# Kernel optimization log

Measured on AMD Instinct MI355X. Metric: run time of the kernel, lower is better.

The kernel has to match this reference:

```python
import jax, jax.numpy as jnp
import numpy as np

B, L, D, H = 1, 2048, 1024, 16
d = D // H  # head dim = 64


def setup_inputs() -> dict:
    key = jax.random.key(0)
    ks = jax.random.split(key, 8)
    s = 1.0 / np.sqrt(D)
    return {
        "x": jax.random.normal(ks[0], (B, L, D), jnp.float32),
        "Wqkv_w": (jax.random.normal(ks[1], (D, 3 * D), jnp.float32) * s),
        "Wqkv_b": jnp.zeros((3 * D,), jnp.float32),
        "out_w": (jax.random.normal(ks[2], (D, D), jnp.float32) * s),
        "out_b": jnp.zeros((D,), jnp.float32),
        "W_static": jnp.zeros((H, d, d), jnp.float32),
        "Lambda_raw": jax.random.uniform(ks[3], (H, d, d), jnp.float32, -3.0, 3.0),
        "Gamma": jax.random.uniform(ks[4], (H, d, d), jnp.float32, -0.5 / np.sqrt(d), 0.5 / np.sqrt(d)),
        "gate_w1": (jax.random.normal(ks[5], (D, D // 2), jnp.float32) * s),
        "gate_b1": jnp.zeros((D // 2,), jnp.float32),
        "gate_w2": (jax.random.normal(ks[6], (D // 2, H), jnp.float32) * (1.0 / np.sqrt(D // 2))),
        "gate_b2": jnp.zeros((H,), jnp.float32),
    }


def _forward(x, Wqkv_w, Wqkv_b, out_w, out_b, W_static, Lambda_raw, Gamma,
             gate_w1, gate_b1, gate_w2, gate_b2):
    Bb, Ll, Dm = x.shape
    Hh = Gamma.shape[0]
    dd = Dm // Hh
    scale = 1.0 / np.sqrt(dd)

    # qkv projection: (B,L,3D) -> (3, B, H, L, d) layout
    qkv = (x @ Wqkv_w + Wqkv_b).reshape(Bb, Ll, 3, Hh, dd)
    q = jnp.transpose(qkv[:, :, 0], (0, 2, 1, 3))  # (B,H,L,d)
    k = jnp.transpose(qkv[:, :, 1], (0, 2, 1, 3))
    v = jnp.transpose(qkv[:, :, 2], (0, 2, 1, 3))

    # --- softmax branch (causal, additive -10000 mask like the original) ---
    scores = jnp.einsum('bhid,bhjd->bhij', q, k) * scale
    causal_mask = jnp.triu(jnp.full((Ll, Ll), -10000.0, dtype=scores.dtype), 1)
    attn = jax.nn.softmax(scores + causal_mask, axis=-1)
    y_softmax = jnp.einsum('bhij,bhjd->bhid', attn, v)

    # --- STP branch: linear recurrence over time via lax.scan ---
    retention = 1.0 - jax.nn.sigmoid(Lambda_raw)  # (H,d,d)
    k_stp = k * scale

    def step(state, inp):
        q_t, k_t, v_t = inp  # each (B,H,d)
        hebbian = v_t[..., :, None] * k_t[..., None, :]          # (B,H,d,d)
        state = retention * state + Gamma * hebbian              # (B,H,d,d)
        y_t = jnp.einsum('bhij,bhj->bhi', W_static + state, q_t)  # (B,H,d)
        return state, y_t

    state0 = jnp.zeros((Bb, Hh, dd, dd), x.dtype)
    qT = jnp.moveaxis(q, 2, 0)      # (L,B,H,d)
    kT = jnp.moveaxis(k_stp, 2, 0)
    vT = jnp.moveaxis(v, 2, 0)
    _, ys = jax.lax.scan(step, state0, (qT, kT, vT))
    y_stp = jnp.moveaxis(ys, 0, 2)  # (B,H,L,d)

    # --- learned gate: Linear -> GELU(exact) -> Linear -> sigmoid ---
    g = jax.nn.gelu(x @ gate_w1 + gate_b1, approximate=False)
    alpha = jax.nn.sigmoid(g @ gate_w2 + gate_b2)        # (B,L,H)
    alpha = jnp.transpose(alpha, (0, 2, 1))[..., None]   # (B,H,L,1)

    y = alpha * y_softmax + (1.0 - alpha) * y_stp        # (B,H,L,d)
    y = jnp.transpose(y, (0, 2, 1, 3)).reshape(Bb, Ll, Dm)
    return y @ out_w + out_b


def reference(x, Wqkv_w, Wqkv_b, out_w, out_b, W_static, Lambda_raw, Gamma,
              gate_w1, gate_b1, gate_w2, gate_b2):
    return _forward(x, Wqkv_w, Wqkv_b, out_w, out_b, W_static, Lambda_raw,
                    Gamma, gate_w1, gate_b1, gate_w2, gate_b2)
```

## Files before the change

### kernel.cpp

```cpp
#include <hip/hip_runtime.h>
#include <hip/hip_bf16.h>

#define L_SEQ 2048
#define DMODEL 1024
#define NHEAD 16
#define DHEAD 64
#define D3 3072

typedef __attribute__((ext_vector_type(8))) short s8v;
typedef __attribute__((ext_vector_type(4))) float f4v;
typedef unsigned int u32;
#define AS1 __attribute__((address_space(1)))
#define AS3 __attribute__((address_space(3)))

__device__ __forceinline__ short f2bf(float f) {
  __hip_bfloat16 h = __float2bfloat16(f);
  return *reinterpret_cast<short*>(&h);
}
__device__ __forceinline__ int pack2bf(float lo, float hi) {
  return (int)(((unsigned)(unsigned short)f2bf(hi) << 16) |
               (unsigned)(unsigned short)f2bf(lo));
}

__global__ __launch_bounds__(256) void conv_x(const float* __restrict__ x,
                                              short* __restrict__ xb)
{
  int i = (blockIdx.x * 256 + threadIdx.x) * 4;
  float4 v = *(const float4*)(x + i);
  short4 o;
  o.x = f2bf(v.x); o.y = f2bf(v.y); o.z = f2bf(v.z); o.w = f2bf(v.w);
  *(short4*)(xb + i) = o;
}

__global__ __launch_bounds__(256) void transpose_conv(const float* __restrict__ W,
    short* __restrict__ Wt, int K, int N)
{
  __shared__ float T[32][33];
  int bx = blockIdx.x, by = blockIdx.y;
  int col = threadIdx.x & 31, rb = threadIdx.x >> 5;
  #pragma unroll
  for (int it = 0; it < 4; ++it) {
    int r = it * 8 + rb;
    T[r][col] = W[(size_t)(by * 32 + r) * N + bx * 32 + col];
  }
  __syncthreads();
  #pragma unroll
  for (int it = 0; it < 4; ++it) {
    int r = it * 8 + rb;
    Wt[(size_t)(bx * 32 + r) * K + by * 32 + col] = f2bf(T[col][r]);
  }
}

__global__ __launch_bounds__(256) void conv_qkv(const float* __restrict__ qkv,
    short* __restrict__ Qb, short* __restrict__ Kb, short* __restrict__ Vtb)
{
  int kb = blockIdx.x, h = blockIdx.y;
  int tid = threadIdx.x;
  __shared__ float Vs[64][65];
  for (int idx = tid; idx < 2048; idx += 256) {
    int key = idx >> 5, e2 = idx & 31;
    size_t base = (size_t)(kb * 64 + key) * D3 + h * 64 + e2 * 2;
    float2 qv = *(const float2*)(qkv + base);
    float2 kv = *(const float2*)(qkv + base + 1024);
    float2 vv = *(const float2*)(qkv + base + 2048);
    size_t o = ((size_t)h * 2048 + kb * 64 + key) * 64 + e2 * 2;
    *(int*)&Qb[o] = pack2bf(qv.x, qv.y);
    *(int*)&Kb[o] = pack2bf(kv.x, kv.y);
    Vs[key][e2 * 2] = vv.x; Vs[key][e2 * 2 + 1] = vv.y;
  }
  __syncthreads();
  for (int idx = tid; idx < 2048; idx += 256) {
    int dim = idx >> 5, k2 = idx & 31;
    *(int*)&Vtb[((size_t)h * 64 + dim) * 2048 + kb * 64 + k2 * 2] =
        pack2bf(Vs[k2 * 2][dim], Vs[k2 * 2 + 1][dim]);
  }
}

template<int BM, int BN, int MODE>
__global__ __launch_bounds__(256) void gemm_mfma(
    const short* __restrict__ A, const short* __restrict__ Bt,
    const float* __restrict__ bias, const float* __restrict__ bias2,
    float* __restrict__ C, short* __restrict__ C2,
    int M, int N, int K)
{
  constexpr int LA = BM / 64, LB = BN / 64;
  constexpr int WM = BM / 2, WN = BN / 2;
  constexpr int MT = WM / 16, NT = WN / 16;
  __shared__ __align__(16) short As[2][BM * 32];
  __shared__ __align__(16) short Bs[2][BN * 32];
  const int tid = threadIdx.x;
  const int w = tid >> 6, lane = tid & 63;
  const int quad = lane >> 4, c = lane & 15;
  const int m0 = blockIdx.y * BM, n0 = blockIdx.x * BN;
  const int wm = (w & 1) * WM, wn = (w >> 1) * WN;
  f4v acc[MT][NT] = {};

  auto stage = [&](int buf, int k0) {
    #pragma unroll
    for (int it = 0; it < LA; ++it) {
      int off = (it * 256 + tid) * 16;
      int row = off >> 6, colh = (off & 63) >> 1;
      __builtin_amdgcn_global_load_lds(
          (const AS1 u32*)(A + (size_t)(m0 + row) * K + k0 + colh),
          (AS3 u32*)(&As[buf][0] + (off >> 1)), 16, 0, 0);
    }
    #pragma unroll
    for (int it = 0; it < LB; ++it) {
      int off = (it * 256 + tid) * 16;
      int row = off >> 6, colh = (off & 63) >> 1;
      __builtin_amdgcn_global_load_lds(
          (const AS1 u32*)(Bt + (size_t)(n0 + row) * K + k0 + colh),
          (AS3 u32*)(&Bs[buf][0] + (off >> 1)), 16, 0, 0);
    }
  };
  stage(0, 0);
  int cur = 0;
  for (int k0 = 0; k0 < K; k0 += 32) {
    __syncthreads();
    if (k0 + 32 < K) stage(cur ^ 1, k0 + 32);
    s8v af[MT], bf[NT];
    #pragma unroll
    for (int mt = 0; mt < MT; ++mt)
      af[mt] = *(s8v*)&As[cur][(wm + mt * 16 + c) * 32 + quad * 8];
    #pragma unroll
    for (int nt = 0; nt < NT; ++nt)
      bf[nt] = *(s8v*)&Bs[cur][(wn + nt * 16 + c) * 32 + quad * 8];
    #pragma unroll
    for (int mt = 0; mt < MT; ++mt)
      #pragma unroll
      for (int nt = 0; nt < NT; ++nt)
        acc[mt][nt] = __builtin_amdgcn_mfma_f32_16x16x32_bf16(
            af[mt], bf[nt], acc[mt][nt], 0, 0, 0);
    cur ^= 1;
  }
  #pragma unroll
  for (int mt = 0; mt < MT; ++mt)
    #pragma unroll
    for (int r = 0; r < 4; ++r) {
      int m = m0 + wm + mt * 16 + quad * 4 + r;
      #pragma unroll
      for (int nt = 0; nt < NT; ++nt) {
        int n = n0 + wn + nt * 16 + c;
        float v = acc[mt][nt][r];
        if (MODE == 0) {
          C[(size_t)m * N + n] = v + bias[n];
        } else {
          if (n < 3072) {
            C[(size_t)m * 3072 + n] = v + bias[n];
          } else {
            float t = v + bias2[n - 3072];
            t = 0.5f * t * (1.0f + erff(t * 0.70710678118654752f));
            C2[(size_t)m * 512 + (n - 3072)] = f2bf(t);
          }
        }
      }
    }
}

__global__ __launch_bounds__(256) void attn_mfma(
    const short* __restrict__ Qb, const short* __restrict__ Kb,
    const short* __restrict__ Vtb, float* __restrict__ ysm)
{
  const int bid = blockIdx.x;
  const int h  = bid & 15;
  const int qt = bid >> 4;
  const int q0 = qt * 64;
  const int nt = qt + 1;
  const int tid = threadIdx.x;
  const int w = tid >> 6, lane = tid & 63;
  const int quad = lane >> 4, c = lane & 15;

  __shared__ __align__(16) char smem[27648];
  short* Ks = (short*)smem;
  short* Vt = Ks + 4608;
  short* Ps = Vt + 4608;
  float* Ob = (float*)smem;

  const int qrow = q0 + w * 16 + c;
  s8v qf[2];
  qf[0] = *(const s8v*)(Qb + ((size_t)h * 2048 + qrow) * 64 + quad * 8);
  qf[1] = *(const s8v*)(Qb + ((size_t)h * 2048 + qrow) * 64 + 32 + quad * 8);

  const int srow = tid >> 3, sc = (tid & 7) * 8;
  int4 pk0, pk1, pv0, pv1;
  auto load_tile = [&](int t0) {
    const short* kbase = Kb + ((size_t)h * 2048 + t0 * 64) * 64;
    const short* vbase = Vtb + (size_t)h * 64 * 2048 + t0 * 64;
    pk0 = *(const int4*)(kbase + (size_t)srow * 64 + sc);
    pk1 = *(const int4*)(kbase + (size_t)(srow + 32) * 64 + sc);
    pv0 = *(const int4*)(vbase + (size_t)srow * 2048 + sc);
    pv1 = *(const int4*)(vbase + (size_t)(srow + 32) * 2048 + sc);
  };
  load_tile(0);

  f4v o_acc[4] = {};
  float m = -1e30f, l = 0.f;

  for (int t0 = 0; t0 < nt; ++t0) {
    __syncthreads();
    *(int4*)&Ks[srow * 72 + sc] = pk0;
    *(int4*)&Ks[(srow + 32) * 72 + sc] = pk1;
    *(int4*)&Vt[srow * 72 + sc] = pv0;
    *(int4*)&Vt[(srow + 32) * 72 + sc] = pv1;
    __syncthreads();
    if (t0 + 1 < nt) load_tile(t0 + 1);

    f4v s_acc[4] = {};
    #pragma unroll
    for (int kt = 0; kt < 4; ++kt) {
      #pragma unroll
      for (int kc = 0; kc < 2; ++kc) {
        s8v kf = *(s8v*)&Ks[(kt * 16 + c) * 72 + kc * 32 + quad * 8];
        s_acc[kt] = __builtin_amdgcn_mfma_f32_16x16x32_bf16(kf, qf[kc], s_acc[kt], 0, 0, 0);
      }
    }
    float sv[4][4];
    bool full = (t0 * 64 + 63) <= (q0 + w * 16);
    #pragma unroll
    for (int kt = 0; kt < 4; ++kt)
      #pragma unroll
      for (int r = 0; r < 4; ++r) {
        float s = s_acc[kt][r] * 0.125f;
        if (!full) {
          int key = t0 * 64 + kt * 16 + quad * 4 + r;
          s = (key <= qrow) ? s : -1e30f;
        }
        sv[kt][r] = s;
      }
    float mloc = -1e30f;
    #pragma unroll
    for (int kt = 0; kt < 4; ++kt)
      #pragma unroll
      for (int r = 0; r < 4; ++r) mloc = fmaxf(mloc, sv[kt][r]);
    mloc = fmaxf(mloc, __shfl_xor(mloc, 16));
    mloc = fmaxf(mloc, __shfl_xor(mloc, 32));
    float mnew = fmaxf(m, mloc);
    float alpha = __expf(m - mnew);
    m = mnew;
    float p[4][4], ls = 0.f;
    #pragma unroll
    for (int kt = 0; kt < 4; ++kt)
      #pragma unroll
      for (int r = 0; r < 4; ++r) { p[kt][r] = __expf(sv[kt][r] - mnew); ls += p[kt][r]; }
    ls += __shfl_xor(ls, 16);
    ls += __shfl_xor(ls, 32);
    l = l * alpha + ls;
    #pragma unroll
    for (int mt = 0; mt < 4; ++mt)
      #pragma unroll
      for (int r = 0; r < 4; ++r) o_acc[mt][r] *= alpha;
    short* Pw = Ps + w * 1152;
    #pragma unroll
    for (int kt = 0; kt < 4; ++kt) {
      *(int*)&Pw[c * 72 + kt * 16 + quad * 4]     = pack2bf(p[kt][0], p[kt][1]);
      *(int*)&Pw[c * 72 + kt * 16 + quad * 4 + 2] = pack2bf(p[kt][2], p[kt][3]);
    }
    #pragma unroll
    for (int kc2 = 0; kc2 < 2; ++kc2) {
      s8v pf = *(s8v*)&Pw[c * 72 + kc2 * 32 + quad * 8];
      #pragma unroll
      for (int mt = 0; mt < 4; ++mt) {
        s8v vf = *(s8v*)&Vt[(mt * 16 + c) * 72 + kc2 * 32 + quad * 8];
        o_acc[mt] = __builtin_amdgcn_mfma_f32_16x16x32_bf16(vf, pf, o_acc[mt], 0, 0, 0);
      }
    }
  }

  float rinv = 1.f / l;
  __syncthreads();
  #pragma unroll
  for (int mt = 0; mt < 4; ++mt)
    #pragma unroll
    for (int r = 0; r < 4; ++r)
      Ob[(w * 16 + c) * 66 + mt * 16 + quad * 4 + r] = o_acc[mt][r] * rinv;
  __syncthreads();
  for (int i = tid; i < 4096; i += 256) {
    int q = i >> 6, e = i & 63;
    ysm[((size_t)h * L_SEQ + q0 + q) * 64 + e] = Ob[q * 66 + e];
  }
}

__global__ __launch_bounds__(256) void stp_local(const float* __restrict__ qkv,
    const float* __restrict__ Lam, const float* __restrict__ Gam,
    float* __restrict__ states)
{
  int c = blockIdx.x, h = blockIdx.y;
  int tid = threadIdx.x;
  int i = tid >> 2, j0 = (tid & 3) * 16;
  __shared__ float Kc[64][64];
  __shared__ float Vc[64][64];
  for (int idx = tid; idx < 64 * 64; idx += 256) {
    int t = idx >> 6, e = idx & 63;
    size_t base = (size_t)(c * 64 + t) * D3 + h * 64 + e;
    Kc[t][e] = qkv[base + 1024] * 0.125f;
    Vc[t][e] = qkv[base + 2048];
  }
  float r[16], g[16], s[16];
  #pragma unroll
  for (int e = 0; e < 16; ++e) {
    int idx = h * 4096 + i * 64 + j0 + e;
    float lam = Lam[idx];
    r[e] = 1.f / (1.f + expf(lam));
    g[e] = Gam[idx];
    s[e] = 0.f;
  }
  __syncthreads();
  for (int t = 0; t < 64; ++t) {
    float v = Vc[t][i];
    #pragma unroll
    for (int e = 0; e < 16; ++e)
      s[e] = r[e] * s[e] + g[e] * (v * Kc[t][j0 + e]);
  }
  #pragma unroll
  for (int e = 0; e < 16; ++e)
    states[((size_t)h * 32 + c) * 4096 + i * 64 + j0 + e] = s[e];
}

__global__ __launch_bounds__(256) void stp_scan(const float* __restrict__ Lam,
                                                float* __restrict__ states)
{
  int gid = blockIdx.x * 256 + threadIdx.x;
  float lam = Lam[gid];
  float r = 1.f / (1.f + expf(lam));
  float r64 = r;
  #pragma unroll
  for (int q = 0; q < 6; ++q) r64 *= r64;
  int h = gid >> 12, low = gid & 4095;
  float acc = 0.f;
  for (int c = 0; c < 32; ++c) {
    size_t idx = ((size_t)h * 32 + c) * 4096 + low;
    float dloc = states[idx];
    states[idx] = acc;
    acc = r64 * acc + dloc;
  }
}

__global__ __launch_bounds__(256) void stp_out(const float* __restrict__ qkv,
    const float* __restrict__ Lam, const float* __restrict__ Gam,
    const float* __restrict__ Wst, const float* __restrict__ states,
    float* __restrict__ ystp)
{
  int c = blockIdx.x, h = blockIdx.y;
  int tid = threadIdx.x;
  int i = tid >> 2, j0 = (tid & 3) * 16;
  __shared__ float Kc[64][64];
  __shared__ float Vc[64][64];
  __shared__ float Qc[64][64];
  for (int idx = tid; idx < 64 * 64; idx += 256) {
    int t = idx >> 6, e = idx & 63;
    size_t base = (size_t)(c * 64 + t) * D3 + h * 64 + e;
    Qc[t][e] = qkv[base];
    Kc[t][e] = qkv[base + 1024] * 0.125f;
    Vc[t][e] = qkv[base + 2048];
  }
  float r[16], g[16], s[16], w[16];
  #pragma unroll
  for (int e = 0; e < 16; ++e) {
    int idx = h * 4096 + i * 64 + j0 + e;
    float lam = Lam[idx];
    r[e] = 1.f / (1.f + expf(lam));
    g[e] = Gam[idx];
    w[e] = Wst[idx];
    s[e] = states[((size_t)h * 32 + c) * 4096 + i * 64 + j0 + e];
  }
  __syncthreads();
  for (int t = 0; t < 64; ++t) {
    float v = Vc[t][i];
    float y = 0.f;
    #pragma unroll
    for (int e = 0; e < 16; ++e) {
      s[e] = r[e] * s[e] + g[e] * (v * Kc[t][j0 + e]);
      y += (w[e] + s[e]) * Qc[t][j0 + e];
    }
    y += __shfl_xor(y, 1);
    y += __shfl_xor(y, 2);
    if ((tid & 3) == 0)
      ystp[((size_t)h * L_SEQ + c * 64 + t) * 64 + i] = y;
  }
}

__global__ __launch_bounds__(256) void gate2_kernel(const short* __restrict__ g_bf,
    const float* __restrict__ w2, const float* __restrict__ b2,
    float* __restrict__ alpha)
{
  int gid = blockIdx.x * 256 + threadIdx.x;
  int l = gid >> 4, h = gid & 15;
  float acc = b2[h];
  const short* grow = g_bf + (size_t)l * 512;
  for (int c2 = 0; c2 < 512; c2 += 2) {
    u32 pk = *(const u32*)(grow + c2);
    float g0 = __uint_as_float(pk << 16);
    float g1 = __uint_as_float(pk & 0xffff0000u);
    acc += g0 * w2[c2 * 16 + h] + g1 * w2[(c2 + 1) * 16 + h];
  }
  alpha[gid] = 1.f / (1.f + expf(-acc));
}

__global__ __launch_bounds__(256) void combine_kernel(const float* __restrict__ ysm,
    const float* __restrict__ ystp, const float* __restrict__ alpha,
    short* __restrict__ ycb)
{
  int gid = blockIdx.x * 256 + threadIdx.x;
  int l = gid >> 10, cidx = gid & 1023;
  int h = cidx >> 6, e = cidx & 63;
  float a = alpha[l * 16 + h];
  size_t src = ((size_t)h * L_SEQ + l) * 64 + e;
  ycb[gid] = f2bf(a * ysm[src] + (1.f - a) * ystp[src]);
}

extern "C" void kernel_launch(void* const* d_in, const int* in_sizes, int n_in,
                              void* d_out, int out_size, void* d_ws, size_t ws_size,
                              hipStream_t stream) {
  (void)in_sizes; (void)n_in; (void)out_size; (void)ws_size;
  const float* x      = (const float*)d_in[0];
  const float* Wqkv_w = (const float*)d_in[1];
  const float* Wqkv_b = (const float*)d_in[2];
  const float* out_w  = (const float*)d_in[3];
  const float* out_b  = (const float*)d_in[4];
  const float* W_st   = (const float*)d_in[5];
  const float* Lam    = (const float*)d_in[6];
  const float* Gam    = (const float*)d_in[7];
  const float* gw1    = (const float*)d_in[8];
  const float* gb1    = (const float*)d_in[9];
  const float* gw2    = (const float*)d_in[10];
  const float* gb2    = (const float*)d_in[11];

  float* ws     = (float*)d_ws;
  float* qkv    = ws;
  float* ysm    = ws + 6291456;
  float* ystp   = ws + 8388608;
  float* states = ws + 10485760;
  float* ovl    = ws + 12582912;
  float* alpha  = ws + 16252928;
  short* xb     = (short*)ovl;
  short* wt_buf = (short*)(ovl + 1048576);
  short* g_bf   = (short*)(ovl + 2883584);
  short* Qb     = (short*)ovl;
  short* Kb     = (short*)(ovl + 1048576);
  short* Vtb    = (short*)(ovl + 2097152);
  short* wtO    = (short*)ovl;
  short* ycb    = (short*)states;

  conv_x<<<dim3(2048), 256, 0, stream>>>(x, xb);
  transpose_conv<<<dim3(96, 32), 256, 0, stream>>>(Wqkv_w, wt_buf, 1024, 3072);
  transpose_conv<<<dim3(16, 32), 256, 0, stream>>>(gw1, wt_buf + 3072 * 1024, 1024, 512);
  gemm_mfma<128, 128, 2><<<dim3(28, 16), 256, 0, stream>>>(
      xb, wt_buf, Wqkv_b, gb1, qkv, g_bf, 2048, 3584, 1024);
  gate2_kernel<<<dim3(128), 256, 0, stream>>>(g_bf, gw2, gb2, alpha);
  stp_local<<<dim3(32, 16), 256, 0, stream>>>(qkv, Lam, Gam, states);
  stp_scan<<<dim3(256), 256, 0, stream>>>(Lam, states);
  stp_out<<<dim3(32, 16), 256, 0, stream>>>(qkv, Lam, Gam, W_st, states, ystp);
  conv_qkv<<<dim3(32, 16), 256, 0, stream>>>(qkv, Qb, Kb, Vtb);
  attn_mfma<<<dim3(512), 256, 0, stream>>>(Qb, Kb, Vtb, ysm);
  combine_kernel<<<dim3(8192), 256, 0, stream>>>(ysm, ystp, alpha, ycb);
  transpose_conv<<<dim3(32, 32), 256, 0, stream>>>(out_w, wtO, 1024, 1024);
  gemm_mfma<64, 128, 0><<<dim3(8, 32), 256, 0, stream>>>(
      ycb, wtO, out_b, nullptr, (float*)d_out, nullptr, 2048, 1024, 1024);
}
```

Before: 275.8 us.

## Split long causal attention rows across two blocks and fuse QK bf16 layout into GEMM

```diff
diff --git a/kernel.cpp b/kernel.cpp
--- a/kernel.cpp
+++ b/kernel.cpp
@@ -17,6 +17,9 @@
   __hip_bfloat16 h = __float2bfloat16(f);
   return *reinterpret_cast<short*>(&h);
 }
+__device__ __forceinline__ float bf2f(short s) {
+  return __uint_as_float(((u32)(unsigned short)s) << 16);
+}
 __device__ __forceinline__ int pack2bf(float lo, float hi) {
   return (int)(((unsigned)(unsigned short)f2bf(hi) << 16) |
                (unsigned)(unsigned short)f2bf(lo));
@@ -51,21 +54,15 @@
   }
 }
 
-__global__ __launch_bounds__(256) void conv_qkv(const float* __restrict__ qkv,
-    short* __restrict__ Qb, short* __restrict__ Kb, short* __restrict__ Vtb)
+__global__ __launch_bounds__(256) void conv_vt(const float* __restrict__ Vf,
+                                               short* __restrict__ Vtb)
 {
   int kb = blockIdx.x, h = blockIdx.y;
   int tid = threadIdx.x;
   __shared__ float Vs[64][65];
   for (int idx = tid; idx < 2048; idx += 256) {
     int key = idx >> 5, e2 = idx & 31;
-    size_t base = (size_t)(kb * 64 + key) * D3 + h * 64 + e2 * 2;
-    float2 qv = *(const float2*)(qkv + base);
-    float2 kv = *(const float2*)(qkv + base + 1024);
-    float2 vv = *(const float2*)(qkv + base + 2048);
-    size_t o = ((size_t)h * 2048 + kb * 64 + key) * 64 + e2 * 2;
-    *(int*)&Qb[o] = pack2bf(qv.x, qv.y);
-    *(int*)&Kb[o] = pack2bf(kv.x, kv.y);
+    float2 vv = *(const float2*)(Vf + (size_t)(kb * 64 + key) * 1024 + h * 64 + e2 * 2);
     Vs[key][e2 * 2] = vv.x; Vs[key][e2 * 2 + 1] = vv.y;
   }
   __syncthreads();
@@ -81,6 +78,7 @@
     const short* __restrict__ A, const short* __restrict__ Bt,
     const float* __restrict__ bias, const float* __restrict__ bias2,
     float* __restrict__ C, short* __restrict__ C2,
+    short* __restrict__ QbP, short* __restrict__ KbP,
     int M, int N, int K)
 {
   constexpr int LA = BM / 64, LB = BN / 64;
@@ -145,8 +143,13 @@
         if (MODE == 0) {
           C[(size_t)m * N + n] = v + bias[n];
         } else {
-          if (n < 3072) {
-            C[(size_t)m * 3072 + n] = v + bias[n];
+          if (n < 2048) {
+            float v2 = v + bias[n];
+            int hh = (n >> 6) & 15, ee = n & 63;
+            short* dst = (n < 1024) ? QbP : KbP;
+            dst[((size_t)hh * 2048 + m) * 64 + ee] = f2bf(v2);
+          } else if (n < 3072) {
+            C[(size_t)m * 1024 + (n - 2048)] = v + bias[n];
           } else {
             float t = v + bias2[n - 3072];
             t = 0.5f * t * (1.0f + erff(t * 0.70710678118654752f));
@@ -159,13 +162,31 @@
 
 __global__ __launch_bounds__(256) void attn_mfma(
     const short* __restrict__ Qb, const short* __restrict__ Kb,
-    const short* __restrict__ Vtb, float* __restrict__ ysm)
+    const short* __restrict__ Vtb, float* __restrict__ O0,
+    float* __restrict__ O1, float* __restrict__ ml)
 {
   const int bid = blockIdx.x;
-  const int h  = bid & 15;
-  const int qt = bid >> 4;
+  int h, qt, ts, te;
+  float *Odst, *mdst, *ldst;
+  if (bid < 512) {
+    qt = 31 - (bid >> 5);
+    int r = bid & 31; h = r >> 1;
+    int n = qt + 1, n2 = (n + 1) >> 1;
+    if ((r & 1) == 0) {
+      ts = 0; te = n2;
+      int s = h * 32 + qt;
+      Odst = O0 + (size_t)s * 4096; mdst = ml + s * 64; ldst = ml + 32768 + s * 64;
+    } else {
+      ts = n2; te = n;
+      int s = h * 16 + (qt - 16);
+      Odst = O1 + (size_t)s * 4096; mdst = ml + 65536 + s * 64; ldst = ml + 81920 + s * 64;
+    }
+  } else {
+    int r = bid - 512; qt = 15 - (r >> 4); h = r & 15; ts = 0; te = qt + 1;
+    int s = h * 32 + qt;
+    Odst = O0 + (size_t)s * 4096; mdst = ml + s * 64; ldst = ml + 32768 + s * 64;
+  }
   const int q0 = qt * 64;
-  const int nt = qt + 1;
   const int tid = threadIdx.x;
   const int w = tid >> 6, lane = tid & 63;
   const int quad = lane >> 4, c = lane & 15;
@@ -191,19 +212,19 @@
     pv0 = *(const int4*)(vbase + (size_t)srow * 2048 + sc);
     pv1 = *(const int4*)(vbase + (size_t)(srow + 32) * 2048 + sc);
   };
-  load_tile(0);
+  load_tile(ts);
 
   f4v o_acc[4] = {};
   float m = -1e30f, l = 0.f;
 
-  for (int t0 = 0; t0 < nt; ++t0) {
+  for (int t0 = ts; t0 < te; ++t0) {
     __syncthreads();
     *(int4*)&Ks[srow * 72 + sc] = pk0;
     *(int4*)&Ks[(srow + 32) * 72 + sc] = pk1;
     *(int4*)&Vt[srow * 72 + sc] = pv0;
     *(int4*)&Vt[(srow + 32) * 72 + sc] = pv1;
     __syncthreads();
-    if (t0 + 1 < nt) load_tile(t0 + 1);
+    if (t0 + 1 < te) load_tile(t0 + 1);
 
     f4v s_acc[4] = {};
     #pragma unroll
@@ -234,7 +255,7 @@
       for (int r = 0; r < 4; ++r) mloc = fmaxf(mloc, sv[kt][r]);
     mloc = fmaxf(mloc, __shfl_xor(mloc, 16));
     mloc = fmaxf(mloc, __shfl_xor(mloc, 32));
-    float mnew = fmaxf(m, mloc);
+    float mnew = fmaxf(fmaxf(m, mloc), -1e20f);
     float alpha = __expf(m - mnew);
     m = mnew;
     float p[4][4], ls = 0.f;
@@ -266,41 +287,76 @@
     }
   }
 
-  float rinv = 1.f / l;
   __syncthreads();
   #pragma unroll
   for (int mt = 0; mt < 4; ++mt)
     #pragma unroll
     for (int r = 0; r < 4; ++r)
-      Ob[(w * 16 + c) * 66 + mt * 16 + quad * 4 + r] = o_acc[mt][r] * rinv;
+      Ob[(w * 16 + c) * 66 + mt * 16 + quad * 4 + r] = o_acc[mt][r];
+  if (quad == 0) { mdst[w * 16 + c] = m; ldst[w * 16 + c] = l; }
   __syncthreads();
-  for (int i = tid; i < 4096; i += 256) {
-    int q = i >> 6, e = i & 63;
-    ysm[((size_t)h * L_SEQ + q0 + q) * 64 + e] = Ob[q * 66 + e];
-  }
-}
-
-__global__ __launch_bounds__(256) void stp_local(const float* __restrict__ qkv,
-    const float* __restrict__ Lam, const float* __restrict__ Gam,
-    float* __restrict__ states)
+  for (int i = tid; i < 4096; i += 256)
+    Odst[i] = Ob[(i >> 6) * 66 + (i & 63)];
+}
+
+__global__ __launch_bounds__(256) void attn_merge(
+    const float* __restrict__ O0, const float* __restrict__ O1,
+    const float* __restrict__ ml, const float* __restrict__ ystp,
+    const float* __restrict__ alpha, short* __restrict__ ycb)
+{
+  int bid = blockIdx.x;
+  int h = bid >> 5, qt = bid & 31;
+  int slot0 = h * 32 + qt;
+  int tid = threadIdx.x;
+  for (int it = 0; it < 16; ++it) {
+    int idx = it * 256 + tid;
+    int q = idx >> 6, e = idx & 63;
+    int gq = qt * 64 + q;
+    float oo = O0[(size_t)slot0 * 4096 + idx];
+    float m0v = ml[slot0 * 64 + q], l0v = ml[32768 + slot0 * 64 + q];
+    float ll;
+    if (qt >= 16) {
+      int slot1 = h * 16 + (qt - 16);
+      float o1 = O1[(size_t)slot1 * 4096 + idx];
+      float m1v = ml[65536 + slot1 * 64 + q], l1v = ml[81920 + slot1 * 64 + q];
+      float ms = fmaxf(m0v, m1v);
+      float w0 = __expf(m0v - ms), w1 = __expf(m1v - ms);
+      oo = oo * w0 + o1 * w1;
+      ll = l0v * w0 + l1v * w1;
+    } else {
+      ll = l0v;
+    }
+    float ys = oo / ll;
+    float a = alpha[gq * 16 + h];
+    float yst = ystp[((size_t)h * 2048 + gq) * 64 + e];
+    ycb[(size_t)gq * 1024 + h * 64 + e] = f2bf(a * ys + (1.f - a) * yst);
+  }
+}
+
+__global__ __launch_bounds__(256) void stp_local(const float* __restrict__ Vf,
+    const short* __restrict__ Kb, const float* __restrict__ Lam,
+    const float* __restrict__ Gam, float* __restrict__ states)
 {
   int c = blockIdx.x, h = blockIdx.y;
   int tid = threadIdx.x;
   int i = tid >> 2, j0 = (tid & 3) * 16;
   __shared__ float Kc[64][64];
   __shared__ float Vc[64][64];
-  for (int idx = tid; idx < 64 * 64; idx += 256) {
-    int t = idx >> 6, e = idx & 63;
-    size_t base = (size_t)(c * 64 + t) * D3 + h * 64 + e;
-    Kc[t][e] = qkv[base + 1024] * 0.125f;
-    Vc[t][e] = qkv[base + 2048];
+  for (int idx = tid; idx < 1024; idx += 256) {
+    int t = idx >> 4, e4 = (idx & 15) * 4;
+    short4 ks = *(const short4*)(Kb + ((size_t)h * 2048 + c * 64 + t) * 64 + e4);
+    Kc[t][e4]     = bf2f(ks.x) * 0.125f;
+    Kc[t][e4 + 1] = bf2f(ks.y) * 0.125f;
+    Kc[t][e4 + 2] = bf2f(ks.z) * 0.125f;
+    Kc[t][e4 + 3] = bf2f(ks.w) * 0.125f;
+    float4 vv = *(const float4*)(Vf + (size_t)(c * 64 + t) * 1024 + h * 64 + e4);
+    Vc[t][e4] = vv.x; Vc[t][e4 + 1] = vv.y; Vc[t][e4 + 2] = vv.z; Vc[t][e4 + 3] = vv.w;
   }
   float r[16], g[16], s[16];
   #pragma unroll
   for (int e = 0; e < 16; ++e) {
     int idx = h * 4096 + i * 64 + j0 + e;
-    float lam = Lam[idx];
-    r[e] = 1.f / (1.f + expf(lam));
+    r[e] = 1.f / (1.f + expf(Lam[idx]));
     g[e] = Gam[idx];
     s[e] = 0.f;
   }
@@ -320,8 +376,7 @@
                                                 float* __restrict__ states)
 {
   int gid = blockIdx.x * 256 + threadIdx.x;
-  float lam = Lam[gid];
-  float r = 1.f / (1.f + expf(lam));
+  float r = 1.f / (1.f + expf(Lam[gid]));
   float r64 = r;
   #pragma unroll
   for (int q = 0; q < 6; ++q) r64 *= r64;
@@ -335,7 +390,8 @@
   }
 }
 
-__global__ __launch_bounds__(256) void stp_out(const float* __restrict__ qkv,
+__global__ __launch_bounds__(256) void stp_out(const float* __restrict__ Vf,
+    const short* __restrict__ Kb, const short* __restrict__ Qb,
     const float* __restrict__ Lam, const float* __restrict__ Gam,
     const float* __restrict__ Wst, const float* __restrict__ states,
     float* __restrict__ ystp)
@@ -346,19 +402,27 @@
   __shared__ float Kc[64][64];
   __shared__ float Vc[64][64];
   __shared__ float Qc[64][64];
-  for (int idx = tid; idx < 64 * 64; idx += 256) {
-    int t = idx >> 6, e = idx & 63;
-    size_t base = (size_t)(c * 64 + t) * D3 + h * 64 + e;
-    Qc[t][e] = qkv[base];
-    Kc[t][e] = qkv[base + 1024] * 0.125f;
-    Vc[t][e] = qkv[base + 2048];
+  for (int idx = tid; idx < 1024; idx += 256) {
+    int t = idx >> 4, e4 = (idx & 15) * 4;
+    size_t bo = ((size_t)h * 2048 + c * 64 + t) * 64 + e4;
+    short4 ks = *(const short4*)(Kb + bo);
+    short4 qs = *(const short4*)(Qb + bo);
+    Kc[t][e4]     = bf2f(ks.x) * 0.125f;
+    Kc[t][e4 + 1] = bf2f(ks.y) * 0.125f;
+    Kc[t][e4 + 2] = bf2f(ks.z) * 0.125f;
+    Kc[t][e4 + 3] = bf2f(ks.w) * 0.125f;
+    Qc[t][e4]     = bf2f(qs.x);
+    Qc[t][e4 + 1] = bf2f(qs.y);
+    Qc[t][e4 + 2] = bf2f(qs.z);
+    Qc[t][e4 + 3] = bf2f(qs.w);
+    float4 vv = *(const float4*)(Vf + (size_t)(c * 64 + t) * 1024 + h * 64 + e4);
+    Vc[t][e4] = vv.x; Vc[t][e4 + 1] = vv.y; Vc[t][e4 + 2] = vv.z; Vc[t][e4 + 3] = vv.w;
   }
   float r[16], g[16], s[16], w[16];
   #pragma unroll
   for (int e = 0; e < 16; ++e) {
     int idx = h * 4096 + i * 64 + j0 + e;
-    float lam = Lam[idx];
-    r[e] = 1.f / (1.f + expf(lam));
+    r[e] = 1.f / (1.f + expf(Lam[idx]));
     g[e] = Gam[idx];
     w[e] = Wst[idx];
     s[e] = states[((size_t)h * 32 + c) * 4096 + i * 64 + j0 + e];
@@ -394,18 +458,6 @@
     acc += g0 * w2[c2 * 16 + h] + g1 * w2[(c2 + 1) * 16 + h];
   }
   alpha[gid] = 1.f / (1.f + expf(-acc));
-}
-
-__global__ __launch_bounds__(256) void combine_kernel(const float* __restrict__ ysm,
-    const float* __restrict__ ystp, const float* __restrict__ alpha,
-    short* __restrict__ ycb)
-{
-  int gid = blockIdx.x * 256 + threadIdx.x;
-  int l = gid >> 10, cidx = gid & 1023;
-  int h = cidx >> 6, e = cidx & 63;
-  float a = alpha[l * 16 + h];
-  size_t src = ((size_t)h * L_SEQ + l) * 64 + e;
-  ycb[gid] = f2bf(a * ysm[src] + (1.f - a) * ystp[src]);
 }
 
 extern "C" void kernel_launch(void* const* d_in, const int* in_sizes, int n_in,
@@ -426,34 +478,36 @@
   const float* gb2    = (const float*)d_in[11];
 
   float* ws     = (float*)d_ws;
-  float* qkv    = ws;
-  float* ysm    = ws + 6291456;
-  float* ystp   = ws + 8388608;
-  float* states = ws + 10485760;
-  float* ovl    = ws + 12582912;
-  float* alpha  = ws + 16252928;
+  float* Vf     = ws;
+  float* O0buf  = ws + 2097152;
+  float* ystp   = ws + 4194304;
+  float* states = ws + 6291456;
+  float* ovl    = ws + 8388608;
+  float* alpha  = ws + 12058624;
+  float* ml     = ws + 12091392;
+  short* Qb     = (short*)(ws + 12189696);
+  short* Kb     = Qb + 2097152;
   short* xb     = (short*)ovl;
   short* wt_buf = (short*)(ovl + 1048576);
   short* g_bf   = (short*)(ovl + 2883584);
-  short* Qb     = (short*)ovl;
-  short* Kb     = (short*)(ovl + 1048576);
-  short* Vtb    = (short*)(ovl + 2097152);
+  short* Vtb    = (short*)ovl;
   short* wtO    = (short*)ovl;
-  short* ycb    = (short*)states;
+  float* O1buf  = states;
+  short* ycb    = (short*)(states + 1048576);
 
   conv_x<<<dim3(2048), 256, 0, stream>>>(x, xb);
   transpose_conv<<<dim3(96, 32), 256, 0, stream>>>(Wqkv_w, wt_buf, 1024, 3072);
   transpose_conv<<<dim3(16, 32), 256, 0, stream>>>(gw1, wt_buf + 3072 * 1024, 1024, 512);
   gemm_mfma<128, 128, 2><<<dim3(28, 16), 256, 0, stream>>>(
-      xb, wt_buf, Wqkv_b, gb1, qkv, g_bf, 2048, 3584, 1024);
+      xb, wt_buf, Wqkv_b, gb1, Vf, g_bf, Qb, Kb, 2048, 3584, 1024);
   gate2_kernel<<<dim3(128), 256, 0, stream>>>(g_bf, gw2, gb2, alpha);
-  stp_local<<<dim3(32, 16), 256, 0, stream>>>(qkv, Lam, Gam, states);
+  stp_local<<<dim3(32, 16), 256, 0, stream>>>(Vf, Kb, Lam, Gam, states);
   stp_scan<<<dim3(256), 256, 0, stream>>>(Lam, states);
-  stp_out<<<dim3(32, 16), 256, 0, stream>>>(qkv, Lam, Gam, W_st, states, ystp);
-  conv_qkv<<<dim3(32, 16), 256, 0, stream>>>(qkv, Qb, Kb, Vtb);
-  attn_mfma<<<dim3(512), 256, 0, stream>>>(Qb, Kb, Vtb, ysm);
-  combine_kernel<<<dim3(8192), 256, 0, stream>>>(ysm, ystp, alpha, ycb);
+  stp_out<<<dim3(32, 16), 256, 0, stream>>>(Vf, Kb, Qb, Lam, Gam, W_st, states, ystp);
+  conv_vt<<<dim3(32, 16), 256, 0, stream>>>(Vf, Vtb);
+  attn_mfma<<<dim3(768), 256, 0, stream>>>(Qb, Kb, Vtb, O0buf, O1buf, ml);
+  attn_merge<<<dim3(512), 256, 0, stream>>>(O0buf, O1buf, ml, ystp, alpha, ycb);
   transpose_conv<<<dim3(32, 32), 256, 0, stream>>>(out_w, wtO, 1024, 1024);
   gemm_mfma<64, 128, 0><<<dim3(8, 32), 256, 0, stream>>>(
-      ycb, wtO, out_b, nullptr, (float*)d_out, nullptr, 2048, 1024, 1024);
-}
+      ycb, wtO, out_b, nullptr, (float*)d_out, nullptr, nullptr, nullptr, 2048, 1024, 1024);
+}
```

Result: no change. 277.8 us (+0.7%).
